# Kernel optimization log

Hardware: AMD Instinct MI355X
Metric: run time of the kernel (lower is better)

## Reference

```python
import jax, jax.numpy as jnp
import numpy as np

V, E, H, L, B = 32000, 128, 32, 64, 32


def setup_inputs() -> dict:
    key = jax.random.key(0)
    k0, k1, k2, k3, k4, k5 = jax.random.split(key, 6)
    stdv = 1.0 / np.sqrt(H)
    we = jax.random.uniform(k0, (V, E), minval=-stdv, maxval=stdv, dtype=jnp.float32)
    we = we.at[1].set(0.0)  # pad token row zeroed, as in original
    i2h1 = jax.random.uniform(k1, (E + H, H), minval=-stdv, maxval=stdv, dtype=jnp.float32)
    i2h2 = jax.random.uniform(k2, (E + H, H), minval=-stdv, maxval=stdv, dtype=jnp.float32)
    h2o = jax.random.uniform(k3, (2 * H, V), minval=-stdv, maxval=stdv, dtype=jnp.float32)
    bias = jnp.ones((1, H), dtype=jnp.float32)  # assigned after reset_parameters -> stays ones
    hidden_init = jax.random.normal(k4, (1, H), dtype=jnp.float32)  # plain buffer, not reset
    inp = jax.random.randint(k5, (L, B), 0, V, dtype=jnp.int64)
    return {"inp": inp, "we": we, "i2h1": i2h1, "i2h2": i2h2,
            "h2o": h2o, "bias": bias, "hidden_init": hidden_init}


def reference(inp, we, i2h1, i2h2, h2o, bias, hidden_init):
    Lr, Br = inp.shape
    Hh = hidden_init.shape[1]
    emb = we[inp]                                   # [L,B,E] embedding gather
    h0 = jnp.broadcast_to(hidden_init, (Br, Hh))    # [B,H]
    b = jnp.broadcast_to(bias, (Br, Hh))            # [B,H]

    def make_step(W):
        def step(h, e):
            h_new = jnp.tanh(jnp.concatenate([e, h], axis=1) @ W + b)
            return h_new, h_new
        return step

    # forward direction: hf[i] = hidden after consuming token i
    _, hf = jax.lax.scan(make_step(i2h1), h0, emb)
    # backward direction (scan over reversed time, flip back)
    _, hb_rev = jax.lax.scan(make_step(i2h2), h0, emb[::-1])
    hb = hb_rev[::-1]                               # hb[i] = bwd hidden after token i

    # original uses hiddenf[i] (pre-token-i fwd state) and hiddenb[i+1] (post-token-(i+1) bwd state)
    hf_used = jnp.concatenate([h0[None], hf[:-1]], axis=0)   # [L,B,H]
    hb_used = jnp.concatenate([hb[1:], h0[None]], axis=0)    # [L,B,H]

    hcat = jnp.concatenate([hf_used, hb_used], axis=-1)      # [L,B,2H]
    logits = jnp.einsum('lbh,hv->lbv', hcat, h2o)            # [L,B,V]
    return jax.nn.log_softmax(logits, axis=-1)
```

## Files before the change

kernel.cpp:

```cpp
#include <hip/hip_runtime.h>

#define V_SZ 32000
#define E_SZ 128
#define H_SZ 32
#define L_SZ 64
#define B_SZ 32
#define M_TOT 2048
#define K2 64
#define NVT 125
#define NMT 32

typedef __bf16 bf16x8 __attribute__((ext_vector_type(8)));
typedef float f32x4 __attribute__((ext_vector_type(4)));

__device__ __forceinline__ unsigned short f2bf(float f) {
    unsigned int u = __float_as_uint(f);
    u += 0x7FFFu + ((u >> 16) & 1u);
    return (unsigned short)(u >> 16);
}

__device__ __forceinline__ void load_bfrag(
    const __bf16* __restrict__ h2oT, int xcol, int wn, int lg, int lr,
    bf16x8 bfr[8][2]) {
    const int colbase = xcol * 256;
#pragma unroll
    for (int n = 0; n < 8; ++n) {
        int col = colbase + wn * 128 + n * 16 + lr;
        const __bf16* bp = h2oT + (size_t)col * K2 + lg * 8;
        bfr[n][0] = *(const bf16x8*)(bp);
        bfr[n][1] = *(const bf16x8*)(bp + 32);
    }
}

__device__ __forceinline__ void tile_gemm(
    const __bf16* __restrict__ hcat, int rowbase, int wm, int lg, int lr,
    const bf16x8 bfr[8][2], f32x4 acc[2][8]) {
    bf16x8 af[2][2];
#pragma unroll
    for (int m = 0; m < 2; ++m) {
        int row = rowbase + wm * 32 + m * 16 + lr;
#pragma unroll
        for (int kh = 0; kh < 2; ++kh)
            af[m][kh] = *(const bf16x8*)(hcat + row * K2 + kh * 32 + lg * 8);
    }
#pragma unroll
    for (int m = 0; m < 2; ++m)
#pragma unroll
        for (int n = 0; n < 8; ++n) acc[m][n] = (f32x4){0.f, 0.f, 0.f, 0.f};
#pragma unroll
    for (int n = 0; n < 8; ++n)
#pragma unroll
        for (int m = 0; m < 2; ++m) {
            acc[m][n] = __builtin_amdgcn_mfma_f32_16x16x32_bf16(af[m][0], bfr[n][0], acc[m][n], 0, 0, 0);
            acc[m][n] = __builtin_amdgcn_mfma_f32_16x16x32_bf16(af[m][1], bfr[n][1], acc[m][n], 0, 0, 0);
        }
}

__global__ __launch_bounds__(256) void k_prep_rnn(
    const int* __restrict__ inp, const float* __restrict__ we,
    const float* __restrict__ i2h1, const float* __restrict__ i2h2,
    const float* __restrict__ h2o, const float* __restrict__ bias,
    const float* __restrict__ hinit,
    unsigned short* __restrict__ hcat_u, unsigned short* __restrict__ h2oT_u) {
    const int tid = threadIdx.x;
    const int p = blockIdx.x;
    if (p < 125) {
        const int v = p * 256 + tid;
        unsigned int* dst = (unsigned int*)(h2oT_u + (size_t)v * K2);
#pragma unroll
        for (int k = 0; k < K2; k += 2) {
            float a = h2o[(size_t)k * V_SZ + v];
            float b = h2o[(size_t)(k + 1) * V_SZ + v];
            dst[k >> 1] = (unsigned int)f2bf(a) | ((unsigned int)f2bf(b) << 16);
        }
        return;
    }
    const int w2 = p - 125;
    const int dir = w2 >> 4;
    const int bpair = w2 & 15;
    const float* W = dir ? i2h2 : i2h1;
    __shared__ float Xl[L_SZ * 2 * H_SZ];
    {
        const int j = tid & 31, bb = (tid >> 5) & 1, to = tid >> 6;
        const int b = bpair * 2 + bb;
        const float bj = bias[j];
        for (int tt = 0; tt < 16; ++tt) {
            const int t = to * 16 + tt;
            const int idx = inp[t * B_SZ + b];
            const float* er = we + (size_t)idx * E_SZ;
            float acc = bj;
#pragma unroll
            for (int k0 = 0; k0 < E_SZ; k0 += 4) {
                f32x4 e4 = *(const f32x4*)(er + k0);
                acc += e4.x * W[(k0 + 0) * H_SZ + j];
                acc += e4.y * W[(k0 + 1) * H_SZ + j];
                acc += e4.z * W[(k0 + 2) * H_SZ + j];
                acc += e4.w * W[(k0 + 3) * H_SZ + j];
            }
            Xl[(t * 2 + bb) * H_SZ + j] = acc;
        }
    }
    __syncthreads();
    if (tid < 64) {
        const int lane = tid;
        const int bb = lane >> 5;
        const int b = bpair * 2 + bb;
        const int j = lane & 31;
        const int srcbase = lane & 32;
        float wh[H_SZ];
#pragma unroll
        for (int k = 0; k < H_SZ; ++k) wh[k] = W[(E_SZ + k) * H_SZ + j];
        float h = hinit[j];
        for (int step = 0; step < L_SZ; ++step) {
            const int tt = dir ? (L_SZ - 1 - step) : step;
            hcat_u[(tt * B_SZ + b) * K2 + dir * H_SZ + j] = f2bf(h);
            float a0 = Xl[(tt * 2 + bb) * H_SZ + j];
            float a1 = 0.f, a2 = 0.f, a3 = 0.f;
#pragma unroll
            for (int k = 0; k < H_SZ; k += 4) {
                a0 += __shfl(h, srcbase | k, 64) * wh[k];
                a1 += __shfl(h, srcbase | (k + 1), 64) * wh[k + 1];
                a2 += __shfl(h, srcbase | (k + 2), 64) * wh[k + 2];
                a3 += __shfl(h, srcbase | (k + 3), 64) * wh[k + 3];
            }
            float x2 = (a0 + a1) + (a2 + a3);
            float e = __expf(2.f * x2);
            h = 1.f - 2.f * __builtin_amdgcn_rcpf(e + 1.f);
        }
    }
}

__global__ __launch_bounds__(256) void k_pass_a(
    const __bf16* __restrict__ hcat, const __bf16* __restrict__ h2oT,
    float* __restrict__ Asum) {
    const int tid = threadIdx.x;
    const int wave = tid >> 6, lane = tid & 63;
    const int wm = wave >> 1, wn = wave & 1;
    const int lg = lane >> 4, lr = lane & 15;
    const int rowbase = blockIdx.y * 64;
    bf16x8 bfr[8][2];
    load_bfrag(h2oT, blockIdx.x, wn, lg, lr, bfr);
    f32x4 acc[2][8];
    tile_gemm(hcat, rowbase, wm, lg, lr, bfr, acc);
    float rs[2][4];
#pragma unroll
    for (int m = 0; m < 2; ++m)
#pragma unroll
        for (int r = 0; r < 4; ++r) {
            float s = 0.f;
#pragma unroll
            for (int n = 0; n < 8; ++n) s += __expf(acc[m][n][r]);
            rs[m][r] = s;
        }
#pragma unroll
    for (int mask = 1; mask < 16; mask <<= 1)
#pragma unroll
        for (int m = 0; m < 2; ++m)
#pragma unroll
            for (int r = 0; r < 4; ++r)
                rs[m][r] += __shfl_xor(rs[m][r], mask, 64);
    __shared__ float tsum[2][64];
    if (lr == 0) {
#pragma unroll
        for (int m = 0; m < 2; ++m)
#pragma unroll
            for (int r = 0; r < 4; ++r)
                tsum[wn][wm * 32 + m * 16 + lg * 4 + r] = rs[m][r];
    }
    __syncthreads();
    if (tid < 64)
        Asum[blockIdx.x * M_TOT + rowbase + tid] = tsum[0][tid] + tsum[1][tid];
}

__global__ __launch_bounds__(256) void k_lse(
    const float* __restrict__ Asum, float* __restrict__ lse) {
    const int row = blockIdx.x * 256 + threadIdx.x;
    float s = 0.f;
    for (int i = 0; i < NVT; ++i) s += Asum[i * M_TOT + row];
    lse[row] = logf(s);
}

__global__ __launch_bounds__(256) void k_pass_b(
    const __bf16* __restrict__ hcat, const __bf16* __restrict__ h2oT,
    const float* __restrict__ lse, float* __restrict__ out) {
    const int tid = threadIdx.x;
    const int wave = tid >> 6, lane = tid & 63;
    const int wm = wave >> 1, wn = wave & 1;
    const int lg = lane >> 4, lr = lane & 15;
    const int rowbase = blockIdx.y * 64;
    const int colbase = blockIdx.x * 256;
    bf16x8 bfr[8][2];
    load_bfrag(h2oT, blockIdx.x, wn, lg, lr, bfr);
    f32x4 acc[2][8];
    tile_gemm(hcat, rowbase, wm, lg, lr, bfr, acc);
    float lsev[2][4];
#pragma unroll
    for (int m = 0; m < 2; ++m)
#pragma unroll
        for (int r = 0; r < 4; ++r)
            lsev[m][r] = lse[rowbase + wm * 32 + m * 16 + lg * 4 + r];
#pragma unroll
    for (int m = 0; m < 2; ++m)
#pragma unroll
        for (int r = 0; r < 4; ++r) {
            const int row = rowbase + wm * 32 + m * 16 + lg * 4 + r;
            float* rp = out + (size_t)row * V_SZ + colbase + wn * 128 + lr;
#pragma unroll
            for (int n = 0; n < 8; ++n)
                rp[n * 16] = acc[m][n][r] - lsev[m][r];
        }
}

extern "C" void kernel_launch(void* const* d_in, const int* in_sizes, int n_in,
                              void* d_out, int out_size, void* d_ws, size_t ws_size,
                              hipStream_t stream) {
    (void)in_sizes; (void)n_in; (void)out_size; (void)ws_size;
    const int*   inp   = (const int*)d_in[0];
    const float* we    = (const float*)d_in[1];
    const float* i2h1  = (const float*)d_in[2];
    const float* i2h2  = (const float*)d_in[3];
    const float* h2o   = (const float*)d_in[4];
    const float* bias  = (const float*)d_in[5];
    const float* hinit = (const float*)d_in[6];
    float* out = (float*)d_out;
    char* ws = (char*)d_ws;
    unsigned short* hcat_u = (unsigned short*)(ws);
    unsigned short* h2oT_u = (unsigned short*)(ws + 262144);
    float*          Asum   = (float*)(ws + 4358144);
    float*          lse    = (float*)(ws + 5382144);

    k_prep_rnn<<<157, 256, 0, stream>>>(inp, we, i2h1, i2h2, h2o, bias, hinit,
                                        hcat_u, h2oT_u);
    k_pass_a<<<dim3(NVT, NMT), 256, 0, stream>>>(
        (const __bf16*)hcat_u, (const __bf16*)h2oT_u, Asum);
    k_lse<<<8, 256, 0, stream>>>(Asum, lse);
    k_pass_b<<<dim3(NVT, NMT), 256, 0, stream>>>(
        (const __bf16*)hcat_u, (const __bf16*)h2oT_u, lse, out);
}
```

Measured before the change: 186.9 us.

## Fuse log-sum-exp reduction into pass B and stream B fragments per column tile

Removes the separate k_lse kernel. Each pass-B block now reduces its 64 rows' partial sums from a row-major Asum buffer (transposed, leading dimension 128) and computes the log itself. The goal is to save one launch and a serial dependency, at the cost of every column block recomputing the same row reductions. Both GEMM kernels also load B fragments and issue MFMAs per n-slice instead of holding all accumulators, which lowers register pressure and may raise occupancy.

```diff
diff --git a/kernel.cpp b/kernel.cpp
--- a/kernel.cpp
+++ b/kernel.cpp
@@ -9,6 +9,7 @@
 #define K2 64
 #define NVT 125
 #define NMT 32
+#define ASUM_LD 128
 
 typedef __bf16 bf16x8 __attribute__((ext_vector_type(8)));
 typedef float f32x4 __attribute__((ext_vector_type(4)));
@@ -17,43 +18,6 @@
     unsigned int u = __float_as_uint(f);
     u += 0x7FFFu + ((u >> 16) & 1u);
     return (unsigned short)(u >> 16);
-}
-
-__device__ __forceinline__ void load_bfrag(
-    const __bf16* __restrict__ h2oT, int xcol, int wn, int lg, int lr,
-    bf16x8 bfr[8][2]) {
-    const int colbase = xcol * 256;
-#pragma unroll
-    for (int n = 0; n < 8; ++n) {
-        int col = colbase + wn * 128 + n * 16 + lr;
-        const __bf16* bp = h2oT + (size_t)col * K2 + lg * 8;
-        bfr[n][0] = *(const bf16x8*)(bp);
-        bfr[n][1] = *(const bf16x8*)(bp + 32);
-    }
-}
-
-__device__ __forceinline__ void tile_gemm(
-    const __bf16* __restrict__ hcat, int rowbase, int wm, int lg, int lr,
-    const bf16x8 bfr[8][2], f32x4 acc[2][8]) {
-    bf16x8 af[2][2];
-#pragma unroll
-    for (int m = 0; m < 2; ++m) {
-        int row = rowbase + wm * 32 + m * 16 + lr;
-#pragma unroll
-        for (int kh = 0; kh < 2; ++kh)
-            af[m][kh] = *(const bf16x8*)(hcat + row * K2 + kh * 32 + lg * 8);
-    }
-#pragma unroll
-    for (int m = 0; m < 2; ++m)
-#pragma unroll
-        for (int n = 0; n < 8; ++n) acc[m][n] = (f32x4){0.f, 0.f, 0.f, 0.f};
-#pragma unroll
-    for (int n = 0; n < 8; ++n)
-#pragma unroll
-        for (int m = 0; m < 2; ++m) {
-            acc[m][n] = __builtin_amdgcn_mfma_f32_16x16x32_bf16(af[m][0], bfr[n][0], acc[m][n], 0, 0, 0);
-            acc[m][n] = __builtin_amdgcn_mfma_f32_16x16x32_bf16(af[m][1], bfr[n][1], acc[m][n], 0, 0, 0);
-        }
 }
 
 __global__ __launch_bounds__(256) void k_prep_rnn(
@@ -138,20 +102,33 @@
     const int wm = wave >> 1, wn = wave & 1;
     const int lg = lane >> 4, lr = lane & 15;
     const int rowbase = blockIdx.y * 64;
-    bf16x8 bfr[8][2];
-    load_bfrag(h2oT, blockIdx.x, wn, lg, lr, bfr);
-    f32x4 acc[2][8];
-    tile_gemm(hcat, rowbase, wm, lg, lr, bfr, acc);
-    float rs[2][4];
-#pragma unroll
-    for (int m = 0; m < 2; ++m)
+    const int colbase = blockIdx.x * 256;
+    bf16x8 af[2][2];
+#pragma unroll
+    for (int m = 0; m < 2; ++m) {
+        int row = rowbase + wm * 32 + m * 16 + lr;
+#pragma unroll
+        for (int kh = 0; kh < 2; ++kh)
+            af[m][kh] = *(const bf16x8*)(hcat + row * K2 + kh * 32 + lg * 8);
+    }
+    float rs[2][4] = {{0.f,0.f,0.f,0.f},{0.f,0.f,0.f,0.f}};
+#pragma unroll
+    for (int n = 0; n < 8; ++n) {
+        const int col = colbase + wn * 128 + n * 16 + lr;
+        const __bf16* bp = h2oT + (size_t)col * K2 + lg * 8;
+        bf16x8 b0 = *(const bf16x8*)(bp);
+        bf16x8 b1 = *(const bf16x8*)(bp + 32);
+        f32x4 a0 = (f32x4){0.f,0.f,0.f,0.f}, a1 = (f32x4){0.f,0.f,0.f,0.f};
+        a0 = __builtin_amdgcn_mfma_f32_16x16x32_bf16(af[0][0], b0, a0, 0, 0, 0);
+        a1 = __builtin_amdgcn_mfma_f32_16x16x32_bf16(af[1][0], b0, a1, 0, 0, 0);
+        a0 = __builtin_amdgcn_mfma_f32_16x16x32_bf16(af[0][1], b1, a0, 0, 0, 0);
+        a1 = __builtin_amdgcn_mfma_f32_16x16x32_bf16(af[1][1], b1, a1, 0, 0, 0);
 #pragma unroll
         for (int r = 0; r < 4; ++r) {
-            float s = 0.f;
-#pragma unroll
-            for (int n = 0; n < 8; ++n) s += __expf(acc[m][n][r]);
-            rs[m][r] = s;
-        }
+            rs[0][r] += __expf(a0[r]);
+            rs[1][r] += __expf(a1[r]);
+        }
+    }
 #pragma unroll
     for (int mask = 1; mask < 16; mask <<= 1)
 #pragma unroll
@@ -169,46 +146,70 @@
     }
     __syncthreads();
     if (tid < 64)
-        Asum[blockIdx.x * M_TOT + rowbase + tid] = tsum[0][tid] + tsum[1][tid];
-}
-
-__global__ __launch_bounds__(256) void k_lse(
-    const float* __restrict__ Asum, float* __restrict__ lse) {
-    const int row = blockIdx.x * 256 + threadIdx.x;
-    float s = 0.f;
-    for (int i = 0; i < NVT; ++i) s += Asum[i * M_TOT + row];
-    lse[row] = logf(s);
+        Asum[(size_t)(rowbase + tid) * ASUM_LD + blockIdx.x] =
+            tsum[0][tid] + tsum[1][tid];
 }
 
 __global__ __launch_bounds__(256) void k_pass_b(
     const __bf16* __restrict__ hcat, const __bf16* __restrict__ h2oT,
-    const float* __restrict__ lse, float* __restrict__ out) {
+    const float* __restrict__ Asum, float* __restrict__ out) {
     const int tid = threadIdx.x;
     const int wave = tid >> 6, lane = tid & 63;
     const int wm = wave >> 1, wn = wave & 1;
     const int lg = lane >> 4, lr = lane & 15;
     const int rowbase = blockIdx.y * 64;
     const int colbase = blockIdx.x * 256;
-    bf16x8 bfr[8][2];
-    load_bfrag(h2oT, blockIdx.x, wn, lg, lr, bfr);
-    f32x4 acc[2][8];
-    tile_gemm(hcat, rowbase, wm, lg, lr, bfr, acc);
+
+    __shared__ float part[64][4];
+    __shared__ float lse_s[64];
+    {
+        const int r = tid >> 2, q = tid & 3;
+        const int i0 = q * 32;
+        const int i1 = (q == 3) ? NVT : (i0 + 32);
+        const float* ap = Asum + (size_t)(rowbase + r) * ASUM_LD;
+        float s = 0.f;
+        for (int i = i0; i < i1; ++i) s += ap[i];
+        part[r][q] = s;
+    }
+    __syncthreads();
+    if (tid < 64)
+        lse_s[tid] = logf(part[tid][0] + part[tid][1] + part[tid][2] + part[tid][3]);
+    __syncthreads();
+
+    bf16x8 af[2][2];
+#pragma unroll
+    for (int m = 0; m < 2; ++m) {
+        int row = rowbase + wm * 32 + m * 16 + lr;
+#pragma unroll
+        for (int kh = 0; kh < 2; ++kh)
+            af[m][kh] = *(const bf16x8*)(hcat + row * K2 + kh * 32 + lg * 8);
+    }
     float lsev[2][4];
 #pragma unroll
     for (int m = 0; m < 2; ++m)
 #pragma unroll
         for (int r = 0; r < 4; ++r)
-            lsev[m][r] = lse[rowbase + wm * 32 + m * 16 + lg * 4 + r];
-#pragma unroll
-    for (int m = 0; m < 2; ++m)
+            lsev[m][r] = lse_s[wm * 32 + m * 16 + lg * 4 + r];
+#pragma unroll
+    for (int n = 0; n < 8; ++n) {
+        const int col = colbase + wn * 128 + n * 16 + lr;
+        const __bf16* bp = h2oT + (size_t)col * K2 + lg * 8;
+        bf16x8 b0 = *(const bf16x8*)(bp);
+        bf16x8 b1 = *(const bf16x8*)(bp + 32);
+        f32x4 a0 = (f32x4){0.f,0.f,0.f,0.f}, a1 = (f32x4){0.f,0.f,0.f,0.f};
+        a0 = __builtin_amdgcn_mfma_f32_16x16x32_bf16(af[0][0], b0, a0, 0, 0, 0);
+        a1 = __builtin_amdgcn_mfma_f32_16x16x32_bf16(af[1][0], b0, a1, 0, 0, 0);
+        a0 = __builtin_amdgcn_mfma_f32_16x16x32_bf16(af[0][1], b1, a0, 0, 0, 0);
+        a1 = __builtin_amdgcn_mfma_f32_16x16x32_bf16(af[1][1], b1, a1, 0, 0, 0);
 #pragma unroll
         for (int r = 0; r < 4; ++r) {
-            const int row = rowbase + wm * 32 + m * 16 + lg * 4 + r;
-            float* rp = out + (size_t)row * V_SZ + colbase + wn * 128 + lr;
-#pragma unroll
-            for (int n = 0; n < 8; ++n)
-                rp[n * 16] = acc[m][n][r] - lsev[m][r];
-        }
+            const int row0 = rowbase + wm * 32 + lg * 4 + r;
+            out[(size_t)(row0)      * V_SZ + colbase + wn * 128 + n * 16 + lr] =
+                a0[r] - lsev[0][r];
+            out[(size_t)(row0 + 16) * V_SZ + colbase + wn * 128 + n * 16 + lr] =
+                a1[r] - lsev[1][r];
+        }
+    }
 }
 
 extern "C" void kernel_launch(void* const* d_in, const int* in_sizes, int n_in,
@@ -227,13 +228,11 @@
     unsigned short* hcat_u = (unsigned short*)(ws);
     unsigned short* h2oT_u = (unsigned short*)(ws + 262144);
     float*          Asum   = (float*)(ws + 4358144);
-    float*          lse    = (float*)(ws + 5382144);
 
     k_prep_rnn<<<157, 256, 0, stream>>>(inp, we, i2h1, i2h2, h2o, bias, hinit,
                                         hcat_u, h2oT_u);
     k_pass_a<<<dim3(NVT, NMT), 256, 0, stream>>>(
         (const __bf16*)hcat_u, (const __bf16*)h2oT_u, Asum);
-    k_lse<<<8, 256, 0, stream>>>(Asum, lse);
     k_pass_b<<<dim3(NVT, NMT), 256, 0, stream>>>(
-        (const __bf16*)hcat_u, (const __bf16*)h2oT_u, lse, out);
-}
+        (const __bf16*)hcat_u, (const __bf16*)h2oT_u, Asum, out);
+}
```

After: 274.9 us. 47.1% more time.

## Transpose MFMA operand roles so output stores become 16-byte vector writes

Applied to the files above, without the earlier changes.

The GEMM now puts the vocabulary dimension in the MFMA A operand and the hidden rows in B. Each lane's accumulator then holds four consecutive vocab columns of one row, so pass B can write the output with 16-byte vector stores instead of scattered 4-byte stores. Each wave now covers 64 rows by 64 columns. Pass A writes per-wave partial sums (500 partitions instead of 125) and drops the shared-memory cross-wave reduction. In exchange, the lse kernel reads four times more partial sums and the workspace grows.

```diff
diff --git a/kernel.cpp b/kernel.cpp
--- a/kernel.cpp
+++ b/kernel.cpp
@@ -9,6 +9,7 @@
 #define K2 64
 #define NVT 125
 #define NMT 32
+#define NPART 500
 
 typedef __bf16 bf16x8 __attribute__((ext_vector_type(8)));
 typedef float f32x4 __attribute__((ext_vector_type(4)));
@@ -19,40 +20,40 @@
     return (unsigned short)(u >> 16);
 }
 
-__device__ __forceinline__ void load_bfrag(
-    const __bf16* __restrict__ h2oT, int xcol, int wn, int lg, int lr,
-    bf16x8 bfr[8][2]) {
-    const int colbase = xcol * 256;
-#pragma unroll
-    for (int n = 0; n < 8; ++n) {
-        int col = colbase + wn * 128 + n * 16 + lr;
-        const __bf16* bp = h2oT + (size_t)col * K2 + lg * 8;
-        bfr[n][0] = *(const bf16x8*)(bp);
-        bfr[n][1] = *(const bf16x8*)(bp + 32);
-    }
-}
-
-__device__ __forceinline__ void tile_gemm(
-    const __bf16* __restrict__ hcat, int rowbase, int wm, int lg, int lr,
-    const bf16x8 bfr[8][2], f32x4 acc[2][8]) {
-    bf16x8 af[2][2];
-#pragma unroll
-    for (int m = 0; m < 2; ++m) {
-        int row = rowbase + wm * 32 + m * 16 + lr;
-#pragma unroll
-        for (int kh = 0; kh < 2; ++kh)
-            af[m][kh] = *(const bf16x8*)(hcat + row * K2 + kh * 32 + lg * 8);
-    }
-#pragma unroll
-    for (int m = 0; m < 2; ++m)
-#pragma unroll
-        for (int n = 0; n < 8; ++n) acc[m][n] = (f32x4){0.f, 0.f, 0.f, 0.f};
-#pragma unroll
-    for (int n = 0; n < 8; ++n)
-#pragma unroll
-        for (int m = 0; m < 2; ++m) {
-            acc[m][n] = __builtin_amdgcn_mfma_f32_16x16x32_bf16(af[m][0], bfr[n][0], acc[m][n], 0, 0, 0);
-            acc[m][n] = __builtin_amdgcn_mfma_f32_16x16x32_bf16(af[m][1], bfr[n][1], acc[m][n], 0, 0, 0);
+__device__ __forceinline__ void load_vfrag(
+    const __bf16* __restrict__ h2oT, int vbase, int lg, int lr,
+    bf16x8 vf[4][2]) {
+#pragma unroll
+    for (int i = 0; i < 4; ++i) {
+        const __bf16* vp = h2oT + (size_t)(vbase + i * 16 + lr) * K2 + lg * 8;
+        vf[i][0] = *(const bf16x8*)(vp);
+        vf[i][1] = *(const bf16x8*)(vp + 32);
+    }
+}
+
+__device__ __forceinline__ void load_hfrag(
+    const __bf16* __restrict__ hcat, int rowbase, int lg, int lr,
+    bf16x8 hf[4][2]) {
+#pragma unroll
+    for (int j = 0; j < 4; ++j) {
+        const __bf16* hp = hcat + (size_t)(rowbase + j * 16 + lr) * K2 + lg * 8;
+        hf[j][0] = *(const bf16x8*)(hp);
+        hf[j][1] = *(const bf16x8*)(hp + 32);
+    }
+}
+
+__device__ __forceinline__ void tile_gemm_t(
+    const bf16x8 vf[4][2], const bf16x8 hf[4][2], f32x4 acc[4][4]) {
+#pragma unroll
+    for (int i = 0; i < 4; ++i)
+#pragma unroll
+        for (int j = 0; j < 4; ++j) acc[i][j] = (f32x4){0.f, 0.f, 0.f, 0.f};
+#pragma unroll
+    for (int i = 0; i < 4; ++i)
+#pragma unroll
+        for (int j = 0; j < 4; ++j) {
+            acc[i][j] = __builtin_amdgcn_mfma_f32_16x16x32_bf16(vf[i][0], hf[j][0], acc[i][j], 0, 0, 0);
+            acc[i][j] = __builtin_amdgcn_mfma_f32_16x16x32_bf16(vf[i][1], hf[j][1], acc[i][j], 0, 0, 0);
         }
 }
 
@@ -135,48 +136,44 @@
     float* __restrict__ Asum) {
     const int tid = threadIdx.x;
     const int wave = tid >> 6, lane = tid & 63;
-    const int wm = wave >> 1, wn = wave & 1;
     const int lg = lane >> 4, lr = lane & 15;
     const int rowbase = blockIdx.y * 64;
-    bf16x8 bfr[8][2];
-    load_bfrag(h2oT, blockIdx.x, wn, lg, lr, bfr);
-    f32x4 acc[2][8];
-    tile_gemm(hcat, rowbase, wm, lg, lr, bfr, acc);
-    float rs[2][4];
-#pragma unroll
-    for (int m = 0; m < 2; ++m)
-#pragma unroll
-        for (int r = 0; r < 4; ++r) {
-            float s = 0.f;
-#pragma unroll
-            for (int n = 0; n < 8; ++n) s += __expf(acc[m][n][r]);
-            rs[m][r] = s;
-        }
-#pragma unroll
-    for (int mask = 1; mask < 16; mask <<= 1)
-#pragma unroll
-        for (int m = 0; m < 2; ++m)
-#pragma unroll
-            for (int r = 0; r < 4; ++r)
-                rs[m][r] += __shfl_xor(rs[m][r], mask, 64);
-    __shared__ float tsum[2][64];
-    if (lr == 0) {
-#pragma unroll
-        for (int m = 0; m < 2; ++m)
-#pragma unroll
-            for (int r = 0; r < 4; ++r)
-                tsum[wn][wm * 32 + m * 16 + lg * 4 + r] = rs[m][r];
-    }
-    __syncthreads();
-    if (tid < 64)
-        Asum[blockIdx.x * M_TOT + rowbase + tid] = tsum[0][tid] + tsum[1][tid];
+    const int vbase = blockIdx.x * 256 + wave * 64;
+
+    bf16x8 vf[4][2], hf[4][2];
+    load_vfrag(h2oT, vbase, lg, lr, vf);
+    load_hfrag(hcat, rowbase, lg, lr, hf);
+    f32x4 acc[4][4];
+    tile_gemm_t(vf, hf, acc);
+
+    float srow[4];
+#pragma unroll
+    for (int j = 0; j < 4; ++j) {
+        float s = 0.f;
+#pragma unroll
+        for (int i = 0; i < 4; ++i)
+#pragma unroll
+            for (int r = 0; r < 4; ++r) s += __expf(acc[i][j][r]);
+        srow[j] = s;
+    }
+#pragma unroll
+    for (int j = 0; j < 4; ++j) {
+        srow[j] += __shfl_xor(srow[j], 16, 64);
+        srow[j] += __shfl_xor(srow[j], 32, 64);
+    }
+    if (lane < 16) {
+        const int pcol = blockIdx.x * 4 + wave;
+#pragma unroll
+        for (int j = 0; j < 4; ++j)
+            Asum[(size_t)pcol * M_TOT + rowbase + j * 16 + lane] = srow[j];
+    }
 }
 
 __global__ __launch_bounds__(256) void k_lse(
     const float* __restrict__ Asum, float* __restrict__ lse) {
     const int row = blockIdx.x * 256 + threadIdx.x;
     float s = 0.f;
-    for (int i = 0; i < NVT; ++i) s += Asum[i * M_TOT + row];
+    for (int i = 0; i < NPART; ++i) s += Asum[(size_t)i * M_TOT + row];
     lse[row] = logf(s);
 }
 
@@ -185,30 +182,34 @@
     const float* __restrict__ lse, float* __restrict__ out) {
     const int tid = threadIdx.x;
     const int wave = tid >> 6, lane = tid & 63;
-    const int wm = wave >> 1, wn = wave & 1;
     const int lg = lane >> 4, lr = lane & 15;
     const int rowbase = blockIdx.y * 64;
-    const int colbase = blockIdx.x * 256;
-    bf16x8 bfr[8][2];
-    load_bfrag(h2oT, blockIdx.x, wn, lg, lr, bfr);
-    f32x4 acc[2][8];
-    tile_gemm(hcat, rowbase, wm, lg, lr, bfr, acc);
-    float lsev[2][4];
-#pragma unroll
-    for (int m = 0; m < 2; ++m)
-#pragma unroll
-        for (int r = 0; r < 4; ++r)
-            lsev[m][r] = lse[rowbase + wm * 32 + m * 16 + lg * 4 + r];
-#pragma unroll
-    for (int m = 0; m < 2; ++m)
-#pragma unroll
-        for (int r = 0; r < 4; ++r) {
-            const int row = rowbase + wm * 32 + m * 16 + lg * 4 + r;
-            float* rp = out + (size_t)row * V_SZ + colbase + wn * 128 + lr;
-#pragma unroll
-            for (int n = 0; n < 8; ++n)
-                rp[n * 16] = acc[m][n][r] - lsev[m][r];
-        }
+    const int vbase = blockIdx.x * 256 + wave * 64;
+
+    bf16x8 vf[4][2], hf[4][2];
+    load_vfrag(h2oT, vbase, lg, lr, vf);
+    load_hfrag(hcat, rowbase, lg, lr, hf);
+    float lsev[4];
+#pragma unroll
+    for (int j = 0; j < 4; ++j)
+        lsev[j] = lse[rowbase + j * 16 + lr];
+
+    f32x4 acc[4][4];
+    tile_gemm_t(vf, hf, acc);
+
+#pragma unroll
+    for (int j = 0; j < 4; ++j) {
+        float* rp = out + (size_t)(rowbase + j * 16 + lr) * V_SZ + vbase + lg * 4;
+#pragma unroll
+        for (int i = 0; i < 4; ++i) {
+            f32x4 v;
+            v.x = acc[i][j].x - lsev[j];
+            v.y = acc[i][j].y - lsev[j];
+            v.z = acc[i][j].z - lsev[j];
+            v.w = acc[i][j].w - lsev[j];
+            *(f32x4*)(rp + i * 16) = v;
+        }
+    }
 }
 
 extern "C" void kernel_launch(void* const* d_in, const int* in_sizes, int n_in,
@@ -227,7 +228,7 @@
     unsigned short* hcat_u = (unsigned short*)(ws);
     unsigned short* h2oT_u = (unsigned short*)(ws + 262144);
     float*          Asum   = (float*)(ws + 4358144);
-    float*          lse    = (float*)(ws + 5382144);
+    float*          lse    = (float*)(ws + 8454144);
 
     k_prep_rnn<<<157, 256, 0, stream>>>(inp, we, i2h1, i2h2, h2o, bias, hinit,
                                         hcat_u, h2oT_u);
```

Result: no change. 190.2 us (+1.8%).
